# Kernel optimization log

Hardware: AMD Instinct MI355X
Metric: run time of the kernel (lower is better)

The kernel has to match this reference:

```python
import jax, jax.numpy as jnp
import numpy as np

B, L = 256, 8192
DIM, NPAT, HIST, WIN = 256, 64, 32, 8


def setup_inputs() -> dict:
    key = jax.random.key(0)
    ks = jax.random.split(key, 6)
    return {
        "x": jax.random.normal(ks[0], (B, L), dtype=jnp.float32),
        "avg_init": jax.random.normal(ks[1], (B, NPAT), dtype=jnp.float32),
        "conv_w": jax.random.normal(ks[2], (DIM, 1, HIST), dtype=jnp.float32) * 0.1,
        "conv_b": jax.random.normal(ks[3], (DIM,), dtype=jnp.float32) * 0.1,
        "keys_w": jax.random.normal(ks[4], (NPAT, DIM), dtype=jnp.float32) * 0.1,
        "shapes_w": jax.random.normal(ks[5], (WIN, NPAT), dtype=jnp.float32) * 0.1,
    }


def reference(x, avg_init, conv_w, conv_b, keys_w, shapes_w):
    b, l = x.shape
    n_pat = keys_w.shape[0]
    hist = conv_w.shape[2]
    win = shapes_w.shape[0]

    # randn avg_scores, centered (module draws fresh randn each forward; we take it as input)
    avg0 = avg_init - jnp.mean(avg_init, axis=-1, keepdims=True)

    padded = jnp.pad(x, ((0, 0), (hist - 1, 0)))[:, None, :]  # [B,1,L+hist-1]
    out = jax.lax.conv_general_dilated(
        padded, conv_w, window_strides=(win,), padding="VALID",
        dimension_numbers=("NCH", "OIH", "NCH"))
    out = out + conv_b[None, :, None]                     # [B,dim,T]
    out = jnp.transpose(out, (2, 0, 1))                   # [T,B,dim]

    # relu6(keys(out)) -> attn scores [T,B,n_pat]
    scores = jnp.clip(jnp.einsum("tbd,pd->tbp", out, keys_w), 0.0, 6.0)

    # sequential balanced-routing scan over T with running average scores
    def step(avg, score):                                 # avg,score: [B,n_pat]
        idx = jnp.argmax(score - avg, axis=-1)
        prob = jax.nn.one_hot(idx, n_pat, dtype=score.dtype)
        return avg + prob - 1.0 / n_pat, prob

    _, probs = jax.lax.scan(step, avg0, scores)           # probs: [T,B,n_pat]
    probs = jnp.transpose(probs, (1, 0, 2))               # [B,T,n_pat]

    signal = jnp.einsum("btp,wp->btw", probs, shapes_w).reshape(b, -1)[:, :l]
    return jax.nn.relu(signal - x)
```

## Files before the change

kernel.cpp:

```cpp
#include <hip/hip_runtime.h>


constexpr int Bb = 256, Ll = 8192, DIMc = 256, NPAT = 64, HIST = 32, WINc = 8;
constexpr int Tt = Ll / WINc;
constexpr int TC = 32;
constexpr int NC = Tt / TC;
constexpr float CINV = 1.0f / 64.0f;

#define DPP_STAGE(m, ctrl, rmask)                                              \
  (m) = fmaxf((m), __int_as_float(__builtin_amdgcn_update_dpp(                 \
            __float_as_int(m), __float_as_int(m), (ctrl), (rmask), 0xF, false)))

#define DPP_ADDF(s, ctrl, rmask)                                               \
  do {                                                                         \
    int _si = __float_as_int(s);                                               \
    int _ti = __builtin_amdgcn_update_dpp(_si, _si, (ctrl), (rmask), 0xF, false); \
    (s) += __int_as_float(_ti);                                                \
  } while (0)

__global__ __launch_bounds__(256) void precompute_kernel(
    const float* __restrict__ conv_w, const float* __restrict__ conv_b,
    const float* __restrict__ keys_w, float* __restrict__ wsf) {
  __shared__ float part[8][32];
  __shared__ float bred[4];
  const int p = blockIdx.x;
  const int t = threadIdx.x;
  const int h = t & 31, g = t >> 5;
  const float* kwp = keys_w + (size_t)p * DIMc;

  float acc = 0.f;
#pragma unroll
  for (int dd = 0; dd < 32; ++dd) {
    int d = g * 32 + dd;
    acc = fmaf(kwp[d], conv_w[d * HIST + h], acc);
  }
  part[g][h] = acc;

  float bp = kwp[t] * conv_b[t];
#pragma unroll
  for (int off = 32; off; off >>= 1) bp += __shfl_down(bp, off);
  if ((t & 63) == 0) bred[t >> 6] = bp;
  __syncthreads();

  if (t < 32) {
    float s = 0.f;
#pragma unroll
    for (int gg = 0; gg < 8; ++gg) s += part[gg][t];
    wsf[(t >> 2) * (NPAT * 4) + p * 4 + (t & 3)] = s;
  } else if (t == 32) {
    wsf[NPAT * HIST + p] = (bred[0] + bred[1]) + (bred[2] + bred[3]);
  }
}

__global__ __launch_bounds__(256) void shaper_kernel(
    const float* __restrict__ x, const float* __restrict__ avg_init,
    const float* __restrict__ shapes_w, const float* __restrict__ wsf,
    float* __restrict__ out) {
  __shared__ __align__(16) float xpad[HIST - 1 + Ll + 1];
  __shared__ float scb[2][TC * NPAT];
  __shared__ unsigned long long idxp[NC * 4];
  __shared__ float shp[WINc * NPAT];

  const int b    = blockIdx.x;
  const int tid  = threadIdx.x;
  const int wid  = tid >> 6;
  const int lane = tid & 63;
  const float* xrow = x + (size_t)b * Ll;

  if (tid < HIST - 1) xpad[tid] = 0.f;
  {
    const float4* xv4 = (const float4*)xrow;
#pragma unroll
    for (int k = 0; k < 8; ++k) {
      int i4 = k * 256 + tid;
      float4 v = xv4[i4];
      float* dst = xpad + HIST - 1 + i4 * 4;
      dst[0] = v.x; dst[1] = v.y; dst[2] = v.z; dst[3] = v.w;
    }
  }
  for (int i = tid; i < WINc * NPAT; i += 256) shp[i] = shapes_w[i];

  float av0;
  {
    float s = avg_init[(size_t)b * NPAT + lane];
    float t = s;
    DPP_ADDF(t, 0xB1, 0xF);
    DPP_ADDF(t, 0x4E, 0xF);
    DPP_ADDF(t, 0x141, 0xF);
    DPP_ADDF(t, 0x140, 0xF);
    DPP_ADDF(t, 0x142, 0xA);
    DPP_ADDF(t, 0x143, 0xC);
    float tot = __int_as_float(__builtin_amdgcn_readlane(__float_as_int(t), 63));
    av0 = s - tot * CINV;
  }

  float4 w2v[8];
  float  b2 = 0.f;
  if (wid > 0) {
    const float4* w2g = (const float4*)wsf;
#pragma unroll
    for (int h4 = 0; h4 < 8; ++h4) w2v[h4] = w2g[h4 * 64 + lane];
    b2 = wsf[NPAT * HIST + lane];
  }
  __syncthreads();

  auto fill = [&](int c, float* __restrict__ sb) {
    int base = c * TC;
    for (int tl = wid - 1; tl < TC; tl += 3) {
      int t = base + tl;
      const float4* xw = (const float4*)(xpad + t * WINc);
      float acc = b2;
#pragma unroll
      for (int h4 = 0; h4 < 8; ++h4) {
        float4 xv = xw[h4];
        float4 wv = w2v[h4];
        acc = fmaf(xv.x, wv.x, acc);
        acc = fmaf(xv.y, wv.y, acc);
        acc = fmaf(xv.z, wv.z, acc);
        acc = fmaf(xv.w, wv.w, acc);
      }
      float sc = fminf(fmaxf(acc, 0.f), 6.f);
      sb[tl * NPAT + lane] = (sc - av0) + (float)t * CINV;
    }
  };

  float C = 0.f;

  auto scan_chunk = [&](const float* __restrict__ sb, int cidx) {
    float U[TC];
#pragma unroll
    for (int i = 0; i < TC; ++i) U[i] = sb[i * NPAT + lane];
    unsigned long long pk0 = 0, pk1 = 0, pk2 = 0, pk3 = 0;
    float v = U[0] - C;
#pragma unroll
    for (int i = 0; i < TC; ++i) {
      float vA = 0.f, vB = 0.f;
      if (i + 1 < TC) { vA = U[i + 1] - C; vB = vA - 1.0f; }
      float m = v;
      DPP_STAGE(m, 0xB1, 0xF);
      DPP_STAGE(m, 0x4E, 0xF);
      DPP_STAGE(m, 0x141, 0xF);
      DPP_STAGE(m, 0x140, 0xF);
      DPP_STAGE(m, 0x142, 0xA);
      DPP_STAGE(m, 0x143, 0xC);
      float gmax = __int_as_float(
          __builtin_amdgcn_readlane(__float_as_int(m), 63));
      bool e = (v == gmax);
      float C1 = C + 1.0f;
      unsigned long long mk = __ballot(e);
      unsigned long long w = (unsigned long long)(__ffsll(mk) - 1);
      if (i < 8)       pk0 |= w << (8 * (i & 7));
      else if (i < 16) pk1 |= w << (8 * (i & 7));
      else if (i < 24) pk2 |= w << (8 * (i & 7));
      else             pk3 |= w << (8 * (i & 7));
      C = e ? C1 : C;
      if (i + 1 < TC) v = e ? vB : vA;
    }
    if (lane == 0) {
      idxp[cidx * 4 + 0] = pk0;
      idxp[cidx * 4 + 1] = pk1;
      idxp[cidx * 4 + 2] = pk2;
      idxp[cidx * 4 + 3] = pk3;
    }
  };

  if (wid > 0) fill(0, scb[0]);
  __syncthreads();

  for (int c = 0; c < NC; ++c) {
    if (wid == 0) {
      scan_chunk(scb[c & 1], c);
    } else if (c + 1 < NC) {
      fill(c + 1, scb[(c + 1) & 1]);
    }
    __syncthreads();
  }

  float4* outv = (float4*)(out + (size_t)b * Ll);
#pragma unroll
  for (int k = 0; k < 8; ++k) {
    int i4 = k * 256 + tid;
    int l0 = i4 * 4;
    int t  = l0 >> 3;
    int w0 = l0 & 7;
    int p  = (int)((idxp[t >> 3] >> (8 * (t & 7))) & 63ull);
    float4 o;
    o.x = fmaxf(shp[(w0 + 0) * NPAT + p] - xpad[HIST - 1 + l0 + 0], 0.f);
    o.y = fmaxf(shp[(w0 + 1) * NPAT + p] - xpad[HIST - 1 + l0 + 1], 0.f);
    o.z = fmaxf(shp[(w0 + 2) * NPAT + p] - xpad[HIST - 1 + l0 + 2], 0.f);
    o.w = fmaxf(shp[(w0 + 3) * NPAT + p] - xpad[HIST - 1 + l0 + 3], 0.f);
    outv[i4] = o;
  }
}

extern "C" void kernel_launch(void* const* d_in, const int* in_sizes, int n_in,
                              void* d_out, int out_size, void* d_ws, size_t ws_size,
                              hipStream_t stream) {
  const float* x        = (const float*)d_in[0];
  const float* avg_init = (const float*)d_in[1];
  const float* conv_w   = (const float*)d_in[2];
  const float* conv_b   = (const float*)d_in[3];
  const float* keys_w   = (const float*)d_in[4];
  const float* shapes_w = (const float*)d_in[5];
  float* wsf = (float*)d_ws;

  precompute_kernel<<<NPAT, 256, 0, stream>>>(conv_w, conv_b, keys_w, wsf);
  shaper_kernel<<<Bb, 256, 0, stream>>>(x, avg_init, shapes_w, wsf,
                                        (float*)d_out);
}
```

Baseline: 169.6 us.

## Speculate argmax two steps ahead using top-two stats to shorten scan critical path

Restructures the sequential routing scan so each step's argmax is computed from top-1/top-2 statistics built before the previous step's winner is known. Because only the previous winner's running count changes between consecutive steps, the next winner can be chosen with scalar selects instead of a full wave reduction on the critical path. It also replaces the row-broadcast DPP stages with permlane16/32 swaps or swizzle/bpermute. The cost is two wave reductions per step instead of one, plus an approximation risk: the winner is taken from top-1/top-2 statistics computed before the previous step's update. Exact floating-point ties and lowest-index tie-breaking may not match the sequential version.

```diff
diff --git a/kernel.cpp b/kernel.cpp
--- a/kernel.cpp
+++ b/kernel.cpp
@@ -17,6 +17,44 @@
     int _ti = __builtin_amdgcn_update_dpp(_si, _si, (ctrl), (rmask), 0xF, false); \
     (s) += __int_as_float(_ti);                                                \
   } while (0)
+
+#if defined(__has_builtin)
+#if __has_builtin(__builtin_amdgcn_permlane16_swap)
+#define HAVE_PL16 1
+#endif
+#if __has_builtin(__builtin_amdgcn_permlane32_swap)
+#define HAVE_PL32 1
+#endif
+#endif
+
+__device__ __forceinline__ float wave_max64(float v, int lane) {
+  float m = v;
+  DPP_STAGE(m, 0xB1, 0xF);
+  DPP_STAGE(m, 0x4E, 0xF);
+  DPP_STAGE(m, 0x141, 0xF);
+  DPP_STAGE(m, 0x140, 0xF);
+#if defined(HAVE_PL16)
+  {
+    auto r = __builtin_amdgcn_permlane16_swap(__float_as_int(m),
+                                              __float_as_int(m), false, false);
+    m = fmaxf(__int_as_float(r[0]), __int_as_float(r[1]));
+  }
+#else
+  m = fmaxf(m, __int_as_float(
+                   __builtin_amdgcn_ds_swizzle(__float_as_int(m), 0x401F)));
+#endif
+#if defined(HAVE_PL32)
+  {
+    auto r = __builtin_amdgcn_permlane32_swap(__float_as_int(m),
+                                              __float_as_int(m), false, false);
+    m = fmaxf(__int_as_float(r[0]), __int_as_float(r[1]));
+  }
+#else
+  m = fmaxf(m, __int_as_float(__builtin_amdgcn_ds_bpermute(
+                   ((lane ^ 32) << 2), __float_as_int(m))));
+#endif
+  return m;
+}
 
 __global__ __launch_bounds__(256) void precompute_kernel(
     const float* __restrict__ conv_w, const float* __restrict__ conv_b,
@@ -125,37 +163,55 @@
   };
 
   float C = 0.f;
+  const float NEGINF = __int_as_float(0xff800000);
 
   auto scan_chunk = [&](const float* __restrict__ sb, int cidx) {
     float U[TC];
 #pragma unroll
     for (int i = 0; i < TC; ++i) U[i] = sb[i * NPAT + lane];
+
     unsigned long long pk0 = 0, pk1 = 0, pk2 = 0, pk3 = 0;
-    float v = U[0] - C;
-#pragma unroll
-    for (int i = 0; i < TC; ++i) {
-      float vA = 0.f, vB = 0.f;
-      if (i + 1 < TC) { vA = U[i + 1] - C; vB = vA - 1.0f; }
-      float m = v;
-      DPP_STAGE(m, 0xB1, 0xF);
-      DPP_STAGE(m, 0x4E, 0xF);
-      DPP_STAGE(m, 0x141, 0xF);
-      DPP_STAGE(m, 0x140, 0xF);
-      DPP_STAGE(m, 0x142, 0xA);
-      DPP_STAGE(m, 0x143, 0xC);
-      float gmax = __int_as_float(
-          __builtin_amdgcn_readlane(__float_as_int(m), 63));
-      bool e = (v == gmax);
-      float C1 = C + 1.0f;
-      unsigned long long mk = __ballot(e);
-      unsigned long long w = (unsigned long long)(__ffsll(mk) - 1);
-      if (i < 8)       pk0 |= w << (8 * (i & 7));
-      else if (i < 16) pk1 |= w << (8 * (i & 7));
-      else if (i < 24) pk2 |= w << (8 * (i & 7));
-      else             pk3 |= w << (8 * (i & 7));
-      C = e ? C1 : C;
-      if (i + 1 < TC) v = e ? vB : vA;
-    }
+
+    auto build_stats = [&](float h, int& wh1o, int& wh2o, bool& gto) {
+      float A  = wave_max64(h, lane);
+      float hm = (h == A) ? NEGINF : h;
+      float Bv = wave_max64(hm, lane);
+      wh1o = __ffsll(__ballot(h == A)) - 1;
+      wh2o = __ffsll(__ballot(hm == Bv)) - 1;
+      gto  = (__ballot(Bv > A - 1.0f) != 0ull);
+    };
+
+    int wh1s[2], wh2s[2];
+    bool gts[2];
+
+    float v0 = U[0] - C;
+    float h1 = U[1] - C;
+    float M0 = wave_max64(v0, lane);
+    build_stats(h1, wh1s[1], wh2s[1], gts[1]);
+    int w = __ffsll(__ballot(v0 == M0)) - 1;
+    C += (lane == w) ? 1.0f : 0.0f;
+    pk0 = (unsigned long long)w;
+    float h2 = U[2] - C;
+    build_stats(h2, wh1s[0], wh2s[0], gts[0]);
+
+#pragma unroll
+    for (int i = 1; i < TC; ++i) {
+      const int p = i & 1;
+      bool rep = (w == wh1s[p]);
+      int  wi  = rep ? (gts[p] ? wh2s[p] : wh1s[p]) : wh1s[p];
+      C += (lane == wi) ? 1.0f : 0.0f;
+      w = wi;
+      unsigned long long wq = (unsigned long long)w;
+      if (i < 8)       pk0 |= wq << (8 * (i & 7));
+      else if (i < 16) pk1 |= wq << (8 * (i & 7));
+      else if (i < 24) pk2 |= wq << (8 * (i & 7));
+      else             pk3 |= wq << (8 * (i & 7));
+      if (i + 2 < TC) {
+        float h = U[i + 2] - C;
+        build_stats(h, wh1s[p], wh2s[p], gts[p]);
+      }
+    }
+
     if (lane == 0) {
       idxp[cidx * 4 + 0] = pk0;
       idxp[cidx * 4 + 1] = pk1;
```

Result: slower. 271.7 us (+60.1%).

## Shorten serial scan critical path with permlane max and deferred argmax extraction

Applied to the files above, without the earlier changes.

The wave-wide max in the sequential routing scan now uses permlane16/32 swaps (with swizzle/bpermute fallbacks), so every lane gets the result directly and the readlane broadcast is dropped. The scan wave no longer does a ballot and first-set-bit per step. It records a per-lane bitmask of the steps where it matched the max, and wave 1 converts these masks to indices for the previous chunk while the next chunk is being scanned. This takes the ballot/ffs work off the serial dependency chain, at the cost of a small double-buffered shared array, extra work in a fill wave, and one final extraction pass.

```diff
diff --git a/kernel.cpp b/kernel.cpp
--- a/kernel.cpp
+++ b/kernel.cpp
@@ -17,6 +17,44 @@
     int _ti = __builtin_amdgcn_update_dpp(_si, _si, (ctrl), (rmask), 0xF, false); \
     (s) += __int_as_float(_ti);                                                \
   } while (0)
+
+#if defined(__has_builtin)
+#if __has_builtin(__builtin_amdgcn_permlane16_swap)
+#define HAVE_PL16 1
+#endif
+#if __has_builtin(__builtin_amdgcn_permlane32_swap)
+#define HAVE_PL32 1
+#endif
+#endif
+
+__device__ __forceinline__ float wave_max64(float v, int lane) {
+  float m = v;
+  DPP_STAGE(m, 0xB1, 0xF);
+  DPP_STAGE(m, 0x4E, 0xF);
+  DPP_STAGE(m, 0x141, 0xF);
+  DPP_STAGE(m, 0x140, 0xF);
+#if defined(HAVE_PL16)
+  {
+    auto r = __builtin_amdgcn_permlane16_swap(__float_as_int(m),
+                                              __float_as_int(m), false, false);
+    m = fmaxf(__int_as_float(r[0]), __int_as_float(r[1]));
+  }
+#else
+  m = fmaxf(m, __int_as_float(
+                   __builtin_amdgcn_ds_swizzle(__float_as_int(m), 0x401F)));
+#endif
+#if defined(HAVE_PL32)
+  {
+    auto r = __builtin_amdgcn_permlane32_swap(__float_as_int(m),
+                                              __float_as_int(m), false, false);
+    m = fmaxf(__int_as_float(r[0]), __int_as_float(r[1]));
+  }
+#else
+  m = fmaxf(m, __int_as_float(__builtin_amdgcn_ds_bpermute(
+                   ((lane ^ 32) << 2), __float_as_int(m))));
+#endif
+  return m;
+}
 
 __global__ __launch_bounds__(256) void precompute_kernel(
     const float* __restrict__ conv_w, const float* __restrict__ conv_b,
@@ -59,6 +97,7 @@
   __shared__ __align__(16) float xpad[HIST - 1 + Ll + 1];
   __shared__ float scb[2][TC * NPAT];
   __shared__ unsigned long long idxp[NC * 4];
+  __shared__ unsigned int bmbuf[2][64];
   __shared__ float shp[WINc * NPAT];
 
   const int b    = blockIdx.x;
@@ -130,37 +169,40 @@
     float U[TC];
 #pragma unroll
     for (int i = 0; i < TC; ++i) U[i] = sb[i * NPAT + lane];
-    unsigned long long pk0 = 0, pk1 = 0, pk2 = 0, pk3 = 0;
+    unsigned int bm = 0u;
     float v = U[0] - C;
 #pragma unroll
     for (int i = 0; i < TC; ++i) {
       float vA = 0.f, vB = 0.f;
       if (i + 1 < TC) { vA = U[i + 1] - C; vB = vA - 1.0f; }
-      float m = v;
-      DPP_STAGE(m, 0xB1, 0xF);
-      DPP_STAGE(m, 0x4E, 0xF);
-      DPP_STAGE(m, 0x141, 0xF);
-      DPP_STAGE(m, 0x140, 0xF);
-      DPP_STAGE(m, 0x142, 0xA);
-      DPP_STAGE(m, 0x143, 0xC);
-      float gmax = __int_as_float(
-          __builtin_amdgcn_readlane(__float_as_int(m), 63));
+      float gmax = wave_max64(v, lane);
       bool e = (v == gmax);
       float C1 = C + 1.0f;
-      unsigned long long mk = __ballot(e);
+      unsigned int bmn = bm | (1u << i);
+      C  = e ? C1 : C;
+      bm = e ? bmn : bm;
+      if (i + 1 < TC) v = e ? vB : vA;
+    }
+    bmbuf[cidx & 1][lane] = bm;
+  };
+
+  auto extract = [&](int cc) {
+    unsigned int bmv = bmbuf[cc & 1][lane];
+    unsigned long long pk0 = 0, pk1 = 0, pk2 = 0, pk3 = 0;
+#pragma unroll
+    for (int i = 0; i < TC; ++i) {
+      unsigned long long mk = __ballot(((bmv >> i) & 1u) != 0u);
       unsigned long long w = (unsigned long long)(__ffsll(mk) - 1);
       if (i < 8)       pk0 |= w << (8 * (i & 7));
       else if (i < 16) pk1 |= w << (8 * (i & 7));
       else if (i < 24) pk2 |= w << (8 * (i & 7));
       else             pk3 |= w << (8 * (i & 7));
-      C = e ? C1 : C;
-      if (i + 1 < TC) v = e ? vB : vA;
     }
     if (lane == 0) {
-      idxp[cidx * 4 + 0] = pk0;
-      idxp[cidx * 4 + 1] = pk1;
-      idxp[cidx * 4 + 2] = pk2;
-      idxp[cidx * 4 + 3] = pk3;
+      idxp[cc * 4 + 0] = pk0;
+      idxp[cc * 4 + 1] = pk1;
+      idxp[cc * 4 + 2] = pk2;
+      idxp[cc * 4 + 3] = pk3;
     }
   };
 
@@ -170,11 +212,14 @@
   for (int c = 0; c < NC; ++c) {
     if (wid == 0) {
       scan_chunk(scb[c & 1], c);
-    } else if (c + 1 < NC) {
-      fill(c + 1, scb[(c + 1) & 1]);
+    } else {
+      if (c + 1 < NC) fill(c + 1, scb[(c + 1) & 1]);
+      if (wid == 1 && c >= 1) extract(c - 1);
     }
     __syncthreads();
   }
+  if (wid == 0) extract(NC - 1);
+  __syncthreads();
 
   float4* outv = (float4*)(out + (size_t)b * Ll);
 #pragma unroll
```

New measurement: 164.2 us. 3.2% less time.

## Pack four patterns per lane in routing scan and defer index extraction

Applied to the files above, without the earlier changes.

The sequential argmax scan now keeps four patterns per lane in one 16-lane row. It reduces each step's max with a local 4-way max plus four DPP stages, with no readlane or ballot. Per-step winners are recorded as per-lane bitmasks, and the other waves decode them into byte indices one chunk later, overlapped with the score fill. This shortens the serial dependency chain per timestep. In exchange, ties now update every tied pattern, and the upper three rows of the wave do redundant work and read past the chunk buffer.

```diff
diff --git a/kernel.cpp b/kernel.cpp
--- a/kernel.cpp
+++ b/kernel.cpp
@@ -57,8 +57,9 @@
     const float* __restrict__ shapes_w, const float* __restrict__ wsf,
     float* __restrict__ out) {
   __shared__ __align__(16) float xpad[HIST - 1 + Ll + 1];
-  __shared__ float scb[2][TC * NPAT];
-  __shared__ unsigned long long idxp[NC * 4];
+  __shared__ __align__(16) float scb[2][TC * NPAT];
+  __shared__ unsigned int bmw[2][4][64];
+  __shared__ unsigned char idx8[Tt];
   __shared__ float shp[WINc * NPAT];
 
   const int b    = blockIdx.x;
@@ -124,43 +125,71 @@
     }
   };
 
-  float C = 0.f;
+  float C0 = 0.f, C1 = 0.f, C2 = 0.f, C3 = 0.f;
 
   auto scan_chunk = [&](const float* __restrict__ sb, int cidx) {
-    float U[TC];
-#pragma unroll
-    for (int i = 0; i < TC; ++i) U[i] = sb[i * NPAT + lane];
-    unsigned long long pk0 = 0, pk1 = 0, pk2 = 0, pk3 = 0;
-    float v = U[0] - C;
+    const float* myp = sb + 4 * lane;
+    float4 ub[4];
+    ub[0] = *(const float4*)(myp + 0 * NPAT);
+    ub[1] = *(const float4*)(myp + 1 * NPAT);
+    ub[2] = *(const float4*)(myp + 2 * NPAT);
+    ub[3] = *(const float4*)(myp + 3 * NPAT);
+    unsigned int bm0 = 0, bm1 = 0, bm2 = 0, bm3 = 0;
+    float v0 = ub[0].x - C0, v1 = ub[0].y - C1;
+    float v2 = ub[0].z - C2, v3 = ub[0].w - C3;
 #pragma unroll
     for (int i = 0; i < TC; ++i) {
-      float vA = 0.f, vB = 0.f;
-      if (i + 1 < TC) { vA = U[i + 1] - C; vB = vA - 1.0f; }
-      float m = v;
-      DPP_STAGE(m, 0xB1, 0xF);
-      DPP_STAGE(m, 0x4E, 0xF);
-      DPP_STAGE(m, 0x141, 0xF);
-      DPP_STAGE(m, 0x140, 0xF);
-      DPP_STAGE(m, 0x142, 0xA);
-      DPP_STAGE(m, 0x143, 0xC);
-      float gmax = __int_as_float(
-          __builtin_amdgcn_readlane(__float_as_int(m), 63));
-      bool e = (v == gmax);
-      float C1 = C + 1.0f;
-      unsigned long long mk = __ballot(e);
-      unsigned long long w = (unsigned long long)(__ffsll(mk) - 1);
-      if (i < 8)       pk0 |= w << (8 * (i & 7));
-      else if (i < 16) pk1 |= w << (8 * (i & 7));
-      else if (i < 24) pk2 |= w << (8 * (i & 7));
-      else             pk3 |= w << (8 * (i & 7));
-      C = e ? C1 : C;
-      if (i + 1 < TC) v = e ? vB : vA;
-    }
-    if (lane == 0) {
-      idxp[cidx * 4 + 0] = pk0;
-      idxp[cidx * 4 + 1] = pk1;
-      idxp[cidx * 4 + 2] = pk2;
-      idxp[cidx * 4 + 3] = pk3;
+      float4 un = ub[(i + 1) & 3];
+      float vA0 = un.x - C0, vA1 = un.y - C1;
+      float vA2 = un.z - C2, vA3 = un.w - C3;
+      float vB0 = vA0 - 1.f, vB1 = vA1 - 1.f;
+      float vB2 = vA2 - 1.f, vB3 = vA3 - 1.f;
+      if (i + 4 < TC)
+        ub[i & 3] = *(const float4*)(myp + (i + 4) * NPAT);
+      float g = fmaxf(fmaxf(v0, v1), fmaxf(v2, v3));
+      DPP_STAGE(g, 0xB1, 0xF);
+      DPP_STAGE(g, 0x4E, 0xF);
+      DPP_STAGE(g, 0x141, 0xF);
+      DPP_STAGE(g, 0x140, 0xF);
+      bool e0 = (v0 == g), e1 = (v1 == g), e2 = (v2 == g), e3 = (v3 == g);
+      unsigned int bit = 1u << i;
+      C0 = e0 ? C0 + 1.f : C0;
+      C1 = e1 ? C1 + 1.f : C1;
+      C2 = e2 ? C2 + 1.f : C2;
+      C3 = e3 ? C3 + 1.f : C3;
+      bm0 = e0 ? (bm0 | bit) : bm0;
+      bm1 = e1 ? (bm1 | bit) : bm1;
+      bm2 = e2 ? (bm2 | bit) : bm2;
+      bm3 = e3 ? (bm3 | bit) : bm3;
+      if (i + 1 < TC) {
+        v0 = e0 ? vB0 : vA0;
+        v1 = e1 ? vB1 : vA1;
+        v2 = e2 ? vB2 : vA2;
+        v3 = e3 ? vB3 : vA3;
+      }
+    }
+    bmw[cidx & 1][0][lane] = bm0;
+    bmw[cidx & 1][1][lane] = bm1;
+    bmw[cidx & 1][2][lane] = bm2;
+    bmw[cidx & 1][3][lane] = bm3;
+  };
+
+  auto extract = [&](int cc) {
+    unsigned int m0 = bmw[cc & 1][0][lane];
+    unsigned int m1 = bmw[cc & 1][1][lane];
+    unsigned int m2 = bmw[cc & 1][2][lane];
+    unsigned int m3 = bmw[cc & 1][3][lane];
+    for (int i = wid - 1; i < TC; i += 3) {
+      unsigned long long k0 = __ballot(((m0 >> i) & 1u) != 0u) & 0xFFFFull;
+      unsigned long long k1 = __ballot(((m1 >> i) & 1u) != 0u) & 0xFFFFull;
+      unsigned long long k2 = __ballot(((m2 >> i) & 1u) != 0u) & 0xFFFFull;
+      unsigned long long k3 = __ballot(((m3 >> i) & 1u) != 0u) & 0xFFFFull;
+      int w = 0;
+      if (k0) w = 4 * (int)(__ffsll(k0) - 1) + 0;
+      if (k1) w = 4 * (int)(__ffsll(k1) - 1) + 1;
+      if (k2) w = 4 * (int)(__ffsll(k2) - 1) + 2;
+      if (k3) w = 4 * (int)(__ffsll(k3) - 1) + 3;
+      if (lane == 0) idx8[cc * TC + i] = (unsigned char)w;
     }
   };
 
@@ -170,11 +199,14 @@
   for (int c = 0; c < NC; ++c) {
     if (wid == 0) {
       scan_chunk(scb[c & 1], c);
-    } else if (c + 1 < NC) {
-      fill(c + 1, scb[(c + 1) & 1]);
+    } else {
+      if (c + 1 < NC) fill(c + 1, scb[(c + 1) & 1]);
+      if (c >= 1) extract(c - 1);
     }
     __syncthreads();
   }
+  if (wid > 0) extract(NC - 1);
+  __syncthreads();
 
   float4* outv = (float4*)(out + (size_t)b * Ll);
 #pragma unroll
@@ -183,7 +215,7 @@
     int l0 = i4 * 4;
     int t  = l0 >> 3;
     int w0 = l0 & 7;
-    int p  = (int)((idxp[t >> 3] >> (8 * (t & 7))) & 63ull);
+    int p  = (int)idx8[t];
     float4 o;
     o.x = fmaxf(shp[(w0 + 0) * NPAT + p] - xpad[HIST - 1 + l0 + 0], 0.f);
     o.y = fmaxf(shp[(w0 + 1) * NPAT + p] - xpad[HIST - 1 + l0 + 1], 0.f);
```

Measured after the change: 191.7 us. 13.0% more time.
